# Kernel optimization log

Measured on AMD Instinct MI355X. Metric: run time of the kernel, lower is better.

## Reference

```python
import jax, jax.numpy as jnp
import numpy as np

N_SAMPLES = 32768
N_MESH = 8
N_VERTS = 50000
N_CHAN = 256
N_LEVELS = 6
DEPTH_VIEW = 2
DEPTH_ALPHA = 2
VIEW_DIM = 3 * 2 * N_LEVELS  # 36


def sincos_embed(x, n_levels):
    # x: (..., 3) -> (..., 3*2*n_levels), ordered [sin(f0*x), cos(f0*x), sin(f1*x), ...]
    freqs = (2.0 ** jnp.arange(n_levels, dtype=x.dtype))  # (L,)
    xf = x[..., None, :] * freqs[:, None]                 # (..., L, 3)
    sc = jnp.stack([jnp.sin(xf), jnp.cos(xf)], axis=-2)   # (..., L, 2, 3)
    return sc.reshape(*x.shape[:-1], n_levels * 2 * 3)


def setup_inputs() -> dict:
    key = jax.random.key(0)
    ks = jax.random.split(key, 20)
    s = N_CHAN ** -0.5
    inp = {
        'verts': jax.random.randint(ks[0], (N_SAMPLES, N_MESH, 3), 0, N_VERTS, dtype=jnp.int64 if jax.config.jax_enable_x64 else jnp.int32),
        'barys': jax.random.uniform(ks[1], (N_SAMPLES, N_MESH, 3), dtype=jnp.float32),
        'views': jax.random.normal(ks[2], (N_SAMPLES, N_MESH, 3), dtype=jnp.float32),
        'emb_tables': jax.random.normal(ks[3], (N_MESH, N_VERTS + 1, N_CHAN), dtype=jnp.float32) * s,
        'w_proj': jax.random.normal(ks[4], (VIEW_DIM, N_CHAN), dtype=jnp.float32) * VIEW_DIM ** -0.5,
        'b_proj': jnp.zeros((N_CHAN,), jnp.float32),
        'view_W': jax.random.normal(ks[5], (DEPTH_VIEW, N_CHAN, N_CHAN), dtype=jnp.float32) * s,
        'view_b': jnp.zeros((DEPTH_VIEW, N_CHAN), jnp.float32),
        'vert_W': jax.random.normal(ks[6], (DEPTH_ALPHA, N_CHAN, N_CHAN), dtype=jnp.float32) * s,
        'vert_b': jnp.zeros((DEPTH_ALPHA, N_CHAN), jnp.float32),
        'alpha_W1': jax.random.normal(ks[7], (N_CHAN, N_CHAN), dtype=jnp.float32) * s,
        'alpha_b1': jnp.zeros((N_CHAN,), jnp.float32),
        'alpha_W2': jax.random.normal(ks[8], (N_CHAN, 1), dtype=jnp.float32) * s,
        'alpha_b2': jnp.zeros((1,), jnp.float32),
        'color_W1': jax.random.normal(ks[9], (2 * N_CHAN, 2 * N_CHAN), dtype=jnp.float32) * (2 * N_CHAN) ** -0.5,
        'color_b1': jnp.zeros((2 * N_CHAN,), jnp.float32),
        'color_W2': jax.random.normal(ks[10], (2 * N_CHAN, 3), dtype=jnp.float32) * (2 * N_CHAN) ** -0.5,
        'color_b2': jnp.zeros((3,), jnp.float32),
    }
    return inp


def reference(verts, barys, views, emb_tables, w_proj, b_proj, view_W, view_b,
              vert_W, vert_b, alpha_W1, alpha_b1, alpha_W2, alpha_b2,
              color_W1, color_b1, color_W2, color_b2):
    idx = verts + 1                                   # (N, M, 3); row 0 reserved
    mesh_ids = jnp.arange(N_MESH)[None, :, None]      # (1, M, 1)
    ve = emb_tables[mesh_ids, idx]                    # (N, M, 3, C) per-mesh gather
    # nn.Embedding max_norm=1.0: renormalize gathered rows with L2 norm > 1
    norm = jnp.linalg.norm(ve, axis=-1, keepdims=True)
    ve = ve * jnp.where(norm > 1.0, 1.0 / jnp.maximum(norm, 1e-7), 1.0)
    # barycentric-weighted sum over the 3 triangle vertices
    vertex_embeds = jnp.einsum('nmv,nmvc->nmc', barys, ve)  # (N, M, C)

    # view branch: sincos -> linear projector -> Linear+ReLU stack
    v = sincos_embed(views, N_LEVELS) @ w_proj + b_proj
    for i in range(DEPTH_VIEW):
        v = jax.nn.relu(v @ view_W[i] + view_b[i])

    # alpha branch: Linear+ReLU stack then identity-activation head
    h = vertex_embeds
    for i in range(DEPTH_ALPHA):
        h = jax.nn.relu(h @ vert_W[i] + vert_b[i])
    alphas = (h @ alpha_W1 + alpha_b1) @ alpha_W2 + alpha_b2  # (N, M, 1)

    # color branch on [view_embed, vertex_embeds], identity activations
    c = jnp.concatenate([v, vertex_embeds], axis=-1)          # (N, M, 2C)
    colors = (c @ color_W1 + color_b1) @ color_W2 + color_b2  # (N, M, 3)

    return jnp.concatenate([colors, alphas], axis=-1)         # (N, M, 4)
```

## Files before the change

kernel.cpp:

```cpp
#include <hip/hip_runtime.h>
#include <math.h>


#define NROWS (32768 * 8)
#define VROWS 50001
#define BM 32

typedef unsigned short u16;
typedef unsigned int u32;
typedef __attribute__((ext_vector_type(8))) short s16x8;
typedef __attribute__((ext_vector_type(4))) float f32x4;

#define MFMA(a, b, c) __builtin_amdgcn_mfma_f32_16x16x32_bf16(a, b, c, 0, 0, 0)

#define WF_OFF 0
#define BL0_OFF 16384
#define AEFF_OFF 16640
#define CEFFT_OFF 16896
#define BA_OFF 18432
#define BC_OFF 18433
#define PK_FLOAT_OFF 18560
#define L0H 0
#define L0L 16384
#define L1H 32768
#define L1L 98304
#define L2H 163840
#define L2L 229376
#define L3H 294912
#define L3L 360448
#define L4H 425984
#define L4L 430080

__device__ __forceinline__ u16 btrunc(float x) { return (u16)(__float_as_uint(x) >> 16); }
__device__ __forceinline__ u16 bround(float x) {
  u32 u = __float_as_uint(x);
  u += 0x7fff + ((u >> 16) & 1);
  return (u16)(u >> 16);
}

__global__ void mc_prep(const float* w_proj, const float* b_proj, const float* view_W,
                        const float* view_b, const float* alpha_W1, const float* alpha_b1,
                        const float* alpha_W2, const float* alpha_b2, const float* color_W1,
                        const float* color_b1, const float* color_W2, const float* color_b2,
                        float* ws) {
  int bid = blockIdx.x, tid = threadIdx.x;
  if (bid < 64) {
    int k = bid, n = tid;
    float s = 0.f;
    if (k < 36)
      for (int j = 0; j < 256; ++j) s = fmaf(w_proj[k * 256 + j], view_W[j * 256 + n], s);
    ws[WF_OFF + k * 256 + n] = s;
  } else if (bid == 64) {
    int n = tid;
    float s = view_b[n];
    for (int j = 0; j < 256; ++j) s = fmaf(b_proj[j], view_W[j * 256 + n], s);
    ws[BL0_OFF + n] = s;
  } else if (bid == 65) {
    int k = tid;
    float s = 0.f;
    for (int j = 0; j < 256; ++j) s = fmaf(alpha_W1[k * 256 + j], alpha_W2[j], s);
    ws[AEFF_OFF + k] = s;
    if (tid == 0) {
      float b = alpha_b2[0];
      for (int j = 0; j < 256; ++j) b = fmaf(alpha_b1[j], alpha_W2[j], b);
      ws[BA_OFF] = b;
    }
  } else {
    int kk = (bid - 66) * 256 + tid;
    for (int c = 0; c < 3; ++c) {
      float s = 0.f;
      for (int j = 0; j < 512; ++j) s = fmaf(color_W1[kk * 512 + j], color_W2[j * 3 + c], s);
      ws[CEFFT_OFF + c * 512 + kk] = s;
    }
    if (bid == 66 && tid == 0) {
      for (int c = 0; c < 3; ++c) {
        float s = color_b2[c];
        for (int j = 0; j < 512; ++j) s = fmaf(color_b1[j], color_W2[j * 3 + c], s);
        ws[BC_OFF + c] = s;
      }
    }
  }
}

__global__ void mc_pack(const float* view_W, const float* vert_W, const float* ws_f, u16* pk) {
  int e = blockIdx.x * 256 + threadIdx.x;
  float x;
  int offh, offl, le;
  if (e < 212992) {
    const float* src;
    int KS;
    if (e < 16384) {
      src = ws_f + WF_OFF; KS = 2; offh = L0H; offl = L0L; le = e;
    } else if (e < 81920) {
      src = view_W + 65536; KS = 8; offh = L1H; offl = L1L; le = e - 16384;
    } else if (e < 147456) {
      src = vert_W; KS = 8; offh = L2H; offl = L2L; le = e - 81920;
    } else {
      src = vert_W + 65536; KS = 8; offh = L3H; offl = L3L; le = e - 147456;
    }
    int j = le & 7, lane = (le >> 3) & 63, rest = le >> 9;
    int ks = rest % KS, at = rest / KS;
    int k = ks * 32 + ((lane >> 4) << 3) + j;
    int n = at * 16 + (lane & 15);
    x = src[k * 256 + n];
  } else {
    le = e - 212992;
    offh = L4H; offl = L4L;
    int j = le & 7, lane = (le >> 3) & 63, ks = le >> 9;
    int k = ks * 32 + ((lane >> 4) << 3) + j;
    int c = lane & 15;
    x = (c < 3) ? ws_f[CEFFT_OFF + c * 512 + 256 + k] : 0.f;
  }
  u16 h = btrunc(x);
  float r = x - __uint_as_float(((u32)h) << 16);
  pk[offh + le] = h;
  pk[offl + le] = btrunc(r);
}

template <int KS, int AS, bool EXTRA, bool BLO>
__device__ __forceinline__ void run_gemm(const u16* Bh, const u16* Bl, const u16* pk,
                                         int offh, int offl, int wid, int lane,
                                         f32x4 (&acc)[4][2], f32x4* accx) {
#pragma unroll
  for (int ks = 0; ks < KS; ++ks) {
    s16x8 b_h[2], b_l[2];
#pragma unroll
    for (int rt = 0; rt < 2; ++rt) {
      int row = rt * 16 + (lane & 15);
      u32 byte = (u32)(row * AS + ks * 64 + ((lane >> 4) << 4));
      byte ^= ((u32)(row & 7) << 4);
      b_h[rt] = *(const s16x8*)((const char*)Bh + byte);
      if (BLO) b_l[rt] = *(const s16x8*)((const char*)Bl + byte);
    }
#pragma unroll
    for (int atl = 0; atl < 4; ++atl) {
      int at = wid * 4 + atl;
      size_t fidx = ((size_t)(at * KS + ks) * 64 + lane) * 8;
      s16x8 a_h = *(const s16x8*)(pk + offh + fidx);
      s16x8 a_l = *(const s16x8*)(pk + offl + fidx);
#pragma unroll
      for (int rt = 0; rt < 2; ++rt) {
        acc[atl][rt] = MFMA(a_h, b_h[rt], acc[atl][rt]);
        if (BLO) acc[atl][rt] = MFMA(a_h, b_l[rt], acc[atl][rt]);
        acc[atl][rt] = MFMA(a_l, b_h[rt], acc[atl][rt]);
      }
    }
    if (EXTRA) {
      if ((ks >> 1) == wid) {
        size_t fx = ((size_t)ks * 64 + lane) * 8;
        s16x8 ax_h = *(const s16x8*)(pk + L4H + fx);
        s16x8 ax_l = *(const s16x8*)(pk + L4L + fx);
#pragma unroll
        for (int rt = 0; rt < 2; ++rt) {
          accx[rt] = MFMA(ax_h, b_h[rt], accx[rt]);
          if (BLO) accx[rt] = MFMA(ax_h, b_l[rt], accx[rt]);
          accx[rt] = MFMA(ax_l, b_h[rt], accx[rt]);
        }
      }
    }
  }
}

__device__ __forceinline__ void zero_acc(f32x4 (&acc)[4][2]) {
#pragma unroll
  for (int a = 0; a < 4; ++a)
#pragma unroll
    for (int r = 0; r < 2; ++r) acc[a][r] = (f32x4){0.f, 0.f, 0.f, 0.f};
}

__device__ __forceinline__ void store_relu(const f32x4 (&acc)[4][2], const float* bias,
                                           u16* Oh, u16* Ol, int wid, int lane) {
  const int lg = (lane >> 4) << 2;
#pragma unroll
  for (int atl = 0; atl < 4; ++atl) {
    int nb = (wid * 4 + atl) * 16 + lg;
    f32x4 bv = *(const f32x4*)(bias + nb);
#pragma unroll
    for (int rt = 0; rt < 2; ++rt) {
      int row = rt * 16 + (lane & 15);
      u32 byte = (u32)(row * 512 + nb * 2);
      byte ^= ((u32)(row & 7) << 4);
      float v0 = acc[atl][rt][0] + bv[0]; v0 = v0 > 0.f ? v0 : 0.f;
      float v1 = acc[atl][rt][1] + bv[1]; v1 = v1 > 0.f ? v1 : 0.f;
      float v2 = acc[atl][rt][2] + bv[2]; v2 = v2 > 0.f ? v2 : 0.f;
      float v3 = acc[atl][rt][3] + bv[3]; v3 = v3 > 0.f ? v3 : 0.f;
      ushort4 h, l;
      float r;
      h.x = btrunc(v0); r = v0 - __uint_as_float(((u32)h.x) << 16); l.x = btrunc(r);
      h.y = btrunc(v1); r = v1 - __uint_as_float(((u32)h.y) << 16); l.y = btrunc(r);
      h.z = btrunc(v2); r = v2 - __uint_as_float(((u32)h.z) << 16); l.z = btrunc(r);
      h.w = btrunc(v3); r = v3 - __uint_as_float(((u32)h.w) << 16); l.w = btrunc(r);
      *(ushort4*)((char*)Oh + byte) = h;
      *(ushort4*)((char*)Ol + byte) = l;
    }
  }
}

__global__ __launch_bounds__(256, 4) void mc_main(const int* __restrict__ verts,
                                                  const float* __restrict__ barys,
                                                  const float* __restrict__ views,
                                                  const float* __restrict__ emb_tables,
                                                  const float* __restrict__ view_b,
                                                  const float* __restrict__ vert_b,
                                                  const float* __restrict__ ws_f,
                                                  const u16* __restrict__ pk,
                                                  float* __restrict__ out) {
  __shared__ u16 ACTh[BM * 256], ACTl[BM * 256];
  __shared__ u16 Eh[BM * 64];
  __shared__ float cpart[4][BM][3];
  __shared__ float apart[4][BM];

  const int tid = threadIdx.x, lane = tid & 63, wid = tid >> 6;
  const int rbase = blockIdx.x * BM;

  for (int p = 0; p < 4; ++p) {
    const int row0 = wid * 8 + p * 2;
    float4 val[2][3];
    float bw[2][3];
#pragma unroll
    for (int r = 0; r < 2; ++r) {
      const int R = rbase + row0 + r;
      const int m = R & 7;
#pragma unroll
      for (int v = 0; v < 3; ++v) {
        int idx = verts[R * 3 + v] + 1;
        bw[r][v] = barys[R * 3 + v];
        val[r][v] = ((const float4*)(emb_tables + ((size_t)m * VROWS + idx) * 256))[lane];
      }
    }
    float ss[2][3];
#pragma unroll
    for (int r = 0; r < 2; ++r)
#pragma unroll
      for (int v = 0; v < 3; ++v)
        ss[r][v] = fmaf(val[r][v].x, val[r][v].x,
                   fmaf(val[r][v].y, val[r][v].y,
                   fmaf(val[r][v].z, val[r][v].z, val[r][v].w * val[r][v].w)));
#pragma unroll
    for (int sh = 1; sh < 64; sh <<= 1) {
#pragma unroll
      for (int r = 0; r < 2; ++r)
#pragma unroll
        for (int v = 0; v < 3; ++v) ss[r][v] += __shfl_xor(ss[r][v], sh);
    }
#pragma unroll
    for (int r = 0; r < 2; ++r) {
      float ax = 0.f, ay = 0.f, az = 0.f, aw = 0.f;
#pragma unroll
      for (int v = 0; v < 3; ++v) {
        float norm = sqrtf(ss[r][v]);
        float scale = norm > 1.f ? 1.f / norm : 1.f;
        float wbs = bw[r][v] * scale;
        ax = fmaf(wbs, val[r][v].x, ax);
        ay = fmaf(wbs, val[r][v].y, ay);
        az = fmaf(wbs, val[r][v].z, az);
        aw = fmaf(wbs, val[r][v].w, aw);
      }
      const int row = row0 + r;
      u32 byte = (u32)(row * 512 + lane * 8);
      byte ^= ((u32)(row & 7) << 4);
      ushort4 h, l;
      float rr;
      h.x = btrunc(ax); rr = ax - __uint_as_float(((u32)h.x) << 16); l.x = btrunc(rr);
      h.y = btrunc(ay); rr = ay - __uint_as_float(((u32)h.y) << 16); l.y = btrunc(rr);
      h.z = btrunc(az); rr = az - __uint_as_float(((u32)h.z) << 16); l.z = btrunc(rr);
      h.w = btrunc(aw); rr = aw - __uint_as_float(((u32)h.w) << 16); l.w = btrunc(rr);
      *(ushort4*)((char*)ACTh + byte) = h;
      *(ushort4*)((char*)ACTl + byte) = l;
    }
  }

  {
    const int row = tid >> 3, slot = tid & 7;
    const int R = rbase + row;
    if (slot < 6) {
      float f = (float)(1 << slot);
#pragma unroll
      for (int d = 0; d < 3; ++d) {
        float x = views[R * 3 + d] * f;
        float s, c;
        sincosf(x, &s, &c);
        u32 b1 = ((u32)(row * 128 + (slot * 6 + d) * 2)) ^ ((u32)(row & 7) << 4);
        u32 b2 = ((u32)(row * 128 + (slot * 6 + 3 + d) * 2)) ^ ((u32)(row & 7) << 4);
        *(u16*)((char*)Eh + b1) = bround(s);
        *(u16*)((char*)Eh + b2) = bround(c);
      }
    } else {
      int c0 = 36 + (slot - 6) * 14;
      for (int c = c0; c < c0 + 14; ++c) {
        u32 b = ((u32)(row * 128 + c * 2)) ^ ((u32)(row & 7) << 4);
        *(u16*)((char*)Eh + b) = 0;
      }
    }
  }
  __syncthreads();

  {
    f32x4 acc[4][2], accx[2];
    zero_acc(acc);
    accx[0] = (f32x4){0.f, 0.f, 0.f, 0.f};
    accx[1] = (f32x4){0.f, 0.f, 0.f, 0.f};
    run_gemm<8, 512, true, true>(ACTh, ACTl, pk, L2H, L2L, wid, lane, acc, accx);
    if ((lane >> 4) == 0) {
#pragma unroll
      for (int rt = 0; rt < 2; ++rt)
#pragma unroll
        for (int c = 0; c < 3; ++c) cpart[wid][rt * 16 + lane][c] = accx[rt][c];
    }
    __syncthreads();
    store_relu(acc, vert_b, ACTh, ACTl, wid, lane);
  }
  __syncthreads();

  {
    f32x4 acc[4][2];
    zero_acc(acc);
    run_gemm<8, 512, false, true>(ACTh, ACTl, pk, L3H, L3L, wid, lane, acc, nullptr);
    const int lg = (lane >> 4) << 2;
    float s[2] = {0.f, 0.f};
#pragma unroll
    for (int atl = 0; atl < 4; ++atl) {
      int nb = (wid * 4 + atl) * 16 + lg;
      f32x4 bv = *(const f32x4*)(vert_b + 256 + nb);
      f32x4 av = *(const f32x4*)(ws_f + AEFF_OFF + nb);
#pragma unroll
      for (int rt = 0; rt < 2; ++rt)
#pragma unroll
        for (int reg = 0; reg < 4; ++reg) {
          float v = acc[atl][rt][reg] + bv[reg];
          v = v > 0.f ? v : 0.f;
          s[rt] = fmaf(v, av[reg], s[rt]);
        }
    }
#pragma unroll
    for (int rt = 0; rt < 2; ++rt) {
      s[rt] += __shfl_xor(s[rt], 16);
      s[rt] += __shfl_xor(s[rt], 32);
    }
    if (lane < 16) {
      apart[wid][lane] = s[0];
      apart[wid][16 + lane] = s[1];
    }
  }
  __syncthreads();

  {
    f32x4 acc[4][2];
    zero_acc(acc);
    run_gemm<2, 128, false, false>(Eh, Eh, pk, L0H, L0L, wid, lane, acc, nullptr);
    store_relu(acc, ws_f + BL0_OFF, ACTh, ACTl, wid, lane);
  }
  __syncthreads();

  {
    f32x4 acc[4][2];
    zero_acc(acc);
    run_gemm<8, 512, false, true>(ACTh, ACTl, pk, L1H, L1L, wid, lane, acc, nullptr);
    const int lg = (lane >> 4) << 2;
    float s[2][3] = {{0.f, 0.f, 0.f}, {0.f, 0.f, 0.f}};
#pragma unroll
    for (int atl = 0; atl < 4; ++atl) {
      int nb = (wid * 4 + atl) * 16 + lg;
      f32x4 bv = *(const f32x4*)(view_b + 256 + nb);
      f32x4 w0 = *(const f32x4*)(ws_f + CEFFT_OFF + 0 * 512 + nb);
      f32x4 w1 = *(const f32x4*)(ws_f + CEFFT_OFF + 1 * 512 + nb);
      f32x4 w2 = *(const f32x4*)(ws_f + CEFFT_OFF + 2 * 512 + nb);
#pragma unroll
      for (int rt = 0; rt < 2; ++rt)
#pragma unroll
        for (int reg = 0; reg < 4; ++reg) {
          float v = acc[atl][rt][reg] + bv[reg];
          v = v > 0.f ? v : 0.f;
          s[rt][0] = fmaf(v, w0[reg], s[rt][0]);
          s[rt][1] = fmaf(v, w1[reg], s[rt][1]);
          s[rt][2] = fmaf(v, w2[reg], s[rt][2]);
        }
    }
#pragma unroll
    for (int rt = 0; rt < 2; ++rt)
#pragma unroll
      for (int c = 0; c < 3; ++c) {
        s[rt][c] += __shfl_xor(s[rt][c], 16);
        s[rt][c] += __shfl_xor(s[rt][c], 32);
      }
    if (lane < 16) {
#pragma unroll
      for (int rt = 0; rt < 2; ++rt)
#pragma unroll
        for (int c = 0; c < 3; ++c) cpart[wid][rt * 16 + lane][c] += s[rt][c];
    }
  }
  __syncthreads();

  if (tid < BM * 4) {
    int row = tid >> 2, c = tid & 3;
    float v;
    if (c < 3) {
      v = cpart[0][row][c] + cpart[1][row][c] + cpart[2][row][c] + cpart[3][row][c] +
          ws_f[BC_OFF + c];
    } else {
      v = apart[0][row] + apart[1][row] + apart[2][row] + apart[3][row] + ws_f[BA_OFF];
    }
    out[(size_t)(rbase + row) * 4 + c] = v;
  }
}

extern "C" void kernel_launch(void* const* d_in, const int* in_sizes, int n_in, void* d_out,
                              int out_size, void* d_ws, size_t ws_size, hipStream_t stream) {
  (void)in_sizes; (void)n_in; (void)out_size; (void)ws_size;
  const int* verts = (const int*)d_in[0];
  const float* barys = (const float*)d_in[1];
  const float* views = (const float*)d_in[2];
  const float* emb_tables = (const float*)d_in[3];
  const float* w_proj = (const float*)d_in[4];
  const float* b_proj = (const float*)d_in[5];
  const float* view_W = (const float*)d_in[6];
  const float* view_b = (const float*)d_in[7];
  const float* vert_W = (const float*)d_in[8];
  const float* vert_b = (const float*)d_in[9];
  const float* alpha_W1 = (const float*)d_in[10];
  const float* alpha_b1 = (const float*)d_in[11];
  const float* alpha_W2 = (const float*)d_in[12];
  const float* alpha_b2 = (const float*)d_in[13];
  const float* color_W1 = (const float*)d_in[14];
  const float* color_b1 = (const float*)d_in[15];
  const float* color_W2 = (const float*)d_in[16];
  const float* color_b2 = (const float*)d_in[17];

  float* ws_f = (float*)d_ws;
  u16* pk = (u16*)(ws_f + PK_FLOAT_OFF);

  mc_prep<<<dim3(68), dim3(256), 0, stream>>>(w_proj, b_proj, view_W, view_b, alpha_W1,
                                              alpha_b1, alpha_W2, alpha_b2, color_W1, color_b1,
                                              color_W2, color_b2, ws_f);
  mc_pack<<<dim3(848), dim3(256), 0, stream>>>(view_W, vert_W, ws_f, pk);
  mc_main<<<dim3(NROWS / BM), dim3(256), 0, stream>>>(verts, barys, views, emb_tables, view_b,
                                                      vert_b, ws_f, pk, (float*)d_out);
}
```

Measured before the change: 983.2 us.

## Double row tile to 64 with 8 waves, batch gathers, atomic LDS reductions

Raises the row tile from 32 to 64 rows and runs 8 waves per block. Each wave now covers 2 output column tiles across 4 row tiles, so every packed weight fragment fetched from global memory is reused across twice as many rows. The embedding gather is restructured to issue 12 loads per batch in two batches, with the sincos encoding placed between them to hide load latency. The per-wave partial sums for color and alpha are replaced by LDS atomicAdd into a single buffer. The trade-offs are higher register pressure under launch bounds of 512 threads, a larger LDS footprint per block and atomic contention in LDS.

```diff
diff --git a/kernel.cpp b/kernel.cpp
--- a/kernel.cpp
+++ b/kernel.cpp
@@ -4,7 +4,8 @@
 
 #define NROWS (32768 * 8)
 #define VROWS 50001
-#define BM 32
+#define BM 64
+#define NW 8
 
 typedef unsigned short u16;
 typedef unsigned int u32;
@@ -120,12 +121,12 @@
 template <int KS, int AS, bool EXTRA, bool BLO>
 __device__ __forceinline__ void run_gemm(const u16* Bh, const u16* Bl, const u16* pk,
                                          int offh, int offl, int wid, int lane,
-                                         f32x4 (&acc)[4][2], f32x4* accx) {
+                                         f32x4 (&acc)[2][4], f32x4* accx) {
 #pragma unroll
   for (int ks = 0; ks < KS; ++ks) {
-    s16x8 b_h[2], b_l[2];
-#pragma unroll
-    for (int rt = 0; rt < 2; ++rt) {
+    s16x8 b_h[4], b_l[4];
+#pragma unroll
+    for (int rt = 0; rt < 4; ++rt) {
       int row = rt * 16 + (lane & 15);
       u32 byte = (u32)(row * AS + ks * 64 + ((lane >> 4) << 4));
       byte ^= ((u32)(row & 7) << 4);
@@ -133,25 +134,25 @@
       if (BLO) b_l[rt] = *(const s16x8*)((const char*)Bl + byte);
     }
 #pragma unroll
-    for (int atl = 0; atl < 4; ++atl) {
-      int at = wid * 4 + atl;
+    for (int atl = 0; atl < 2; ++atl) {
+      int at = wid * 2 + atl;
       size_t fidx = ((size_t)(at * KS + ks) * 64 + lane) * 8;
       s16x8 a_h = *(const s16x8*)(pk + offh + fidx);
       s16x8 a_l = *(const s16x8*)(pk + offl + fidx);
 #pragma unroll
-      for (int rt = 0; rt < 2; ++rt) {
+      for (int rt = 0; rt < 4; ++rt) {
         acc[atl][rt] = MFMA(a_h, b_h[rt], acc[atl][rt]);
         if (BLO) acc[atl][rt] = MFMA(a_h, b_l[rt], acc[atl][rt]);
         acc[atl][rt] = MFMA(a_l, b_h[rt], acc[atl][rt]);
       }
     }
     if (EXTRA) {
-      if ((ks >> 1) == wid) {
+      if (ks == wid) {
         size_t fx = ((size_t)ks * 64 + lane) * 8;
         s16x8 ax_h = *(const s16x8*)(pk + L4H + fx);
         s16x8 ax_l = *(const s16x8*)(pk + L4L + fx);
 #pragma unroll
-        for (int rt = 0; rt < 2; ++rt) {
+        for (int rt = 0; rt < 4; ++rt) {
           accx[rt] = MFMA(ax_h, b_h[rt], accx[rt]);
           if (BLO) accx[rt] = MFMA(ax_h, b_l[rt], accx[rt]);
           accx[rt] = MFMA(ax_l, b_h[rt], accx[rt]);
@@ -161,22 +162,22 @@
   }
 }
 
-__device__ __forceinline__ void zero_acc(f32x4 (&acc)[4][2]) {
-#pragma unroll
-  for (int a = 0; a < 4; ++a)
-#pragma unroll
-    for (int r = 0; r < 2; ++r) acc[a][r] = (f32x4){0.f, 0.f, 0.f, 0.f};
-}
-
-__device__ __forceinline__ void store_relu(const f32x4 (&acc)[4][2], const float* bias,
+__device__ __forceinline__ void zero_acc(f32x4 (&acc)[2][4]) {
+#pragma unroll
+  for (int a = 0; a < 2; ++a)
+#pragma unroll
+    for (int r = 0; r < 4; ++r) acc[a][r] = (f32x4){0.f, 0.f, 0.f, 0.f};
+}
+
+__device__ __forceinline__ void store_relu(const f32x4 (&acc)[2][4], const float* bias,
                                            u16* Oh, u16* Ol, int wid, int lane) {
   const int lg = (lane >> 4) << 2;
 #pragma unroll
-  for (int atl = 0; atl < 4; ++atl) {
-    int nb = (wid * 4 + atl) * 16 + lg;
+  for (int atl = 0; atl < 2; ++atl) {
+    int nb = (wid * 2 + atl) * 16 + lg;
     f32x4 bv = *(const f32x4*)(bias + nb);
 #pragma unroll
-    for (int rt = 0; rt < 2; ++rt) {
+    for (int rt = 0; rt < 4; ++rt) {
       int row = rt * 16 + (lane & 15);
       u32 byte = (u32)(row * 512 + nb * 2);
       byte ^= ((u32)(row & 7) << 4);
@@ -196,7 +197,7 @@
   }
 }
 
-__global__ __launch_bounds__(256, 4) void mc_main(const int* __restrict__ verts,
+__global__ __launch_bounds__(512, 4) void mc_main(const int* __restrict__ verts,
                                                   const float* __restrict__ barys,
                                                   const float* __restrict__ views,
                                                   const float* __restrict__ emb_tables,
@@ -207,105 +208,127 @@
                                                   float* __restrict__ out) {
   __shared__ u16 ACTh[BM * 256], ACTl[BM * 256];
   __shared__ u16 Eh[BM * 64];
-  __shared__ float cpart[4][BM][3];
-  __shared__ float apart[4][BM];
+  __shared__ float cpart[BM * 4];
 
   const int tid = threadIdx.x, lane = tid & 63, wid = tid >> 6;
   const int rbase = blockIdx.x * BM;
 
-  for (int p = 0; p < 4; ++p) {
-    const int row0 = wid * 8 + p * 2;
-    float4 val[2][3];
-    float bw[2][3];
-#pragma unroll
-    for (int r = 0; r < 2; ++r) {
-      const int R = rbase + row0 + r;
-      const int m = R & 7;
+  if (tid < BM * 4) cpart[tid] = 0.f;
+
+  {
+    const int r0 = wid * 8;
+    int idxs[8][3];
+    float bws[8][3];
+#pragma unroll
+    for (int r = 0; r < 8; ++r)
 #pragma unroll
       for (int v = 0; v < 3; ++v) {
-        int idx = verts[R * 3 + v] + 1;
-        bw[r][v] = barys[R * 3 + v];
-        val[r][v] = ((const float4*)(emb_tables + ((size_t)m * VROWS + idx) * 256))[lane];
-      }
-    }
-    float ss[2][3];
-#pragma unroll
-    for (int r = 0; r < 2; ++r)
+        const int R = rbase + r0 + r;
+        idxs[r][v] = verts[R * 3 + v] + 1;
+        bws[r][v] = barys[R * 3 + v];
+      }
+    float4 valA[4][3];
+#pragma unroll
+    for (int r = 0; r < 4; ++r) {
+      const int m = (rbase + r0 + r) & 7;
 #pragma unroll
       for (int v = 0; v < 3; ++v)
-        ss[r][v] = fmaf(val[r][v].x, val[r][v].x,
-                   fmaf(val[r][v].y, val[r][v].y,
-                   fmaf(val[r][v].z, val[r][v].z, val[r][v].w * val[r][v].w)));
-#pragma unroll
-    for (int sh = 1; sh < 64; sh <<= 1) {
-#pragma unroll
-      for (int r = 0; r < 2; ++r)
-#pragma unroll
-        for (int v = 0; v < 3; ++v) ss[r][v] += __shfl_xor(ss[r][v], sh);
-    }
-#pragma unroll
-    for (int r = 0; r < 2; ++r) {
-      float ax = 0.f, ay = 0.f, az = 0.f, aw = 0.f;
-#pragma unroll
-      for (int v = 0; v < 3; ++v) {
-        float norm = sqrtf(ss[r][v]);
-        float scale = norm > 1.f ? 1.f / norm : 1.f;
-        float wbs = bw[r][v] * scale;
-        ax = fmaf(wbs, val[r][v].x, ax);
-        ay = fmaf(wbs, val[r][v].y, ay);
-        az = fmaf(wbs, val[r][v].z, az);
-        aw = fmaf(wbs, val[r][v].w, aw);
-      }
-      const int row = row0 + r;
-      u32 byte = (u32)(row * 512 + lane * 8);
-      byte ^= ((u32)(row & 7) << 4);
-      ushort4 h, l;
-      float rr;
-      h.x = btrunc(ax); rr = ax - __uint_as_float(((u32)h.x) << 16); l.x = btrunc(rr);
-      h.y = btrunc(ay); rr = ay - __uint_as_float(((u32)h.y) << 16); l.y = btrunc(rr);
-      h.z = btrunc(az); rr = az - __uint_as_float(((u32)h.z) << 16); l.z = btrunc(rr);
-      h.w = btrunc(aw); rr = aw - __uint_as_float(((u32)h.w) << 16); l.w = btrunc(rr);
-      *(ushort4*)((char*)ACTh + byte) = h;
-      *(ushort4*)((char*)ACTl + byte) = l;
-    }
-  }
+        valA[r][v] =
+            ((const float4*)(emb_tables + ((size_t)m * VROWS + idxs[r][v]) * 256))[lane];
+    }
+
+    {
+      const int row = tid >> 3, slot = tid & 7;
+      const int R = rbase + row;
+      if (slot < 6) {
+        float f = (float)(1 << slot);
+#pragma unroll
+        for (int d = 0; d < 3; ++d) {
+          float x = views[R * 3 + d] * f;
+          float s, c;
+          sincosf(x, &s, &c);
+          u32 b1 = ((u32)(row * 128 + (slot * 6 + d) * 2)) ^ ((u32)(row & 7) << 4);
+          u32 b2 = ((u32)(row * 128 + (slot * 6 + 3 + d) * 2)) ^ ((u32)(row & 7) << 4);
+          *(u16*)((char*)Eh + b1) = bround(s);
+          *(u16*)((char*)Eh + b2) = bround(c);
+        }
+      } else {
+        int c0 = 36 + (slot - 6) * 14;
+        for (int c = c0; c < c0 + 14; ++c) {
+          u32 b = ((u32)(row * 128 + c * 2)) ^ ((u32)(row & 7) << 4);
+          *(u16*)((char*)Eh + b) = 0;
+        }
+      }
+    }
+
+    float4 valB[4][3];
+#pragma unroll
+    for (int r = 0; r < 4; ++r) {
+      const int m = (rbase + r0 + 4 + r) & 7;
+#pragma unroll
+      for (int v = 0; v < 3; ++v)
+        valB[r][v] =
+            ((const float4*)(emb_tables + ((size_t)m * VROWS + idxs[4 + r][v]) * 256))[lane];
+    }
+
+#define CONSUME(VAL, RBASE_R)                                                                \
+    {                                                                                        \
+      float ss[4][3];                                                                        \
+      _Pragma("unroll") for (int r = 0; r < 4; ++r) _Pragma("unroll") for (int v = 0; v < 3; \
+                                                                           ++v) ss[r][v] =   \
+          fmaf(VAL[r][v].x, VAL[r][v].x,                                                     \
+               fmaf(VAL[r][v].y, VAL[r][v].y,                                                \
+                    fmaf(VAL[r][v].z, VAL[r][v].z, VAL[r][v].w * VAL[r][v].w)));             \
+      _Pragma("unroll") for (int sh = 1; sh < 64; sh <<= 1) {                                \
+        _Pragma("unroll") for (int r = 0; r < 4; ++r) _Pragma("unroll") for (int v = 0;      \
+                                                                             v < 3; ++v)     \
+            ss[r][v] += __shfl_xor(ss[r][v], sh);                                            \
+      }                                                                                      \
+      _Pragma("unroll") for (int r = 0; r < 4; ++r) {                                        \
+        float ax = 0.f, ay = 0.f, az = 0.f, aw = 0.f;                                        \
+        _Pragma("unroll") for (int v = 0; v < 3; ++v) {                                      \
+          float norm = sqrtf(ss[r][v]);                                                      \
+          float scale = norm > 1.f ? 1.f / norm : 1.f;                                       \
+          float wbs = bws[RBASE_R][v] * scale;                                               \
+          ax = fmaf(wbs, VAL[r][v].x, ax);                                                   \
+          ay = fmaf(wbs, VAL[r][v].y, ay);                                                   \
+          az = fmaf(wbs, VAL[r][v].z, az);                                                   \
+          aw = fmaf(wbs, VAL[r][v].w, aw);                                                   \
+        }                                                                                    \
+        const int row = r0 + (RBASE_R);                                                      \
+        u32 byte = (u32)(row * 512 + lane * 8);                                              \
+        byte ^= ((u32)(row & 7) << 4);                                                       \
+        ushort4 h, l;                                                                        \
+        float rr;                                                                            \
+        h.x = btrunc(ax); rr = ax - __uint_as_float(((u32)h.x) << 16); l.x = btrunc(rr);     \
+        h.y = btrunc(ay); rr = ay - __uint_as_float(((u32)h.y) << 16); l.y = btrunc(rr);     \
+        h.z = btrunc(az); rr = az - __uint_as_float(((u32)h.z) << 16); l.z = btrunc(rr);     \
+        h.w = btrunc(aw); rr = aw - __uint_as_float(((u32)h.w) << 16); l.w = btrunc(rr);     \
+        *(ushort4*)((char*)ACTh + byte) = h;                                                 \
+        *(ushort4*)((char*)ACTl + byte) = l;                                                 \
+      }                                                                                      \
+    }
+
+    CONSUME(valA, r)
+#define RPLUS4 (r + 4)
+    CONSUME(valB, RPLUS4)
+#undef RPLUS4
+#undef CONSUME
+  }
+  __syncthreads();
 
   {
-    const int row = tid >> 3, slot = tid & 7;
-    const int R = rbase + row;
-    if (slot < 6) {
-      float f = (float)(1 << slot);
-#pragma unroll
-      for (int d = 0; d < 3; ++d) {
-        float x = views[R * 3 + d] * f;
-        float s, c;
-        sincosf(x, &s, &c);
-        u32 b1 = ((u32)(row * 128 + (slot * 6 + d) * 2)) ^ ((u32)(row & 7) << 4);
-        u32 b2 = ((u32)(row * 128 + (slot * 6 + 3 + d) * 2)) ^ ((u32)(row & 7) << 4);
-        *(u16*)((char*)Eh + b1) = bround(s);
-        *(u16*)((char*)Eh + b2) = bround(c);
-      }
-    } else {
-      int c0 = 36 + (slot - 6) * 14;
-      for (int c = c0; c < c0 + 14; ++c) {
-        u32 b = ((u32)(row * 128 + c * 2)) ^ ((u32)(row & 7) << 4);
-        *(u16*)((char*)Eh + b) = 0;
-      }
-    }
-  }
-  __syncthreads();
-
-  {
-    f32x4 acc[4][2], accx[2];
+    f32x4 acc[2][4], accx[4];
     zero_acc(acc);
-    accx[0] = (f32x4){0.f, 0.f, 0.f, 0.f};
-    accx[1] = (f32x4){0.f, 0.f, 0.f, 0.f};
+#pragma unroll
+    for (int rt = 0; rt < 4; ++rt) accx[rt] = (f32x4){0.f, 0.f, 0.f, 0.f};
     run_gemm<8, 512, true, true>(ACTh, ACTl, pk, L2H, L2L, wid, lane, acc, accx);
-    if ((lane >> 4) == 0) {
-#pragma unroll
-      for (int rt = 0; rt < 2; ++rt)
-#pragma unroll
-        for (int c = 0; c < 3; ++c) cpart[wid][rt * 16 + lane][c] = accx[rt][c];
+    if (lane < 16) {
+#pragma unroll
+      for (int rt = 0; rt < 4; ++rt)
+#pragma unroll
+        for (int c = 0; c < 3; ++c)
+          atomicAdd(&cpart[(rt * 16 + lane) * 4 + c], accx[rt][c]);
     }
     __syncthreads();
     store_relu(acc, vert_b, ACTh, ACTl, wid, lane);
@@ -313,18 +336,18 @@
   __syncthreads();
 
   {
-    f32x4 acc[4][2];
+    f32x4 acc[2][4];
     zero_acc(acc);
     run_gemm<8, 512, false, true>(ACTh, ACTl, pk, L3H, L3L, wid, lane, acc, nullptr);
     const int lg = (lane >> 4) << 2;
-    float s[2] = {0.f, 0.f};
-#pragma unroll
-    for (int atl = 0; atl < 4; ++atl) {
-      int nb = (wid * 4 + atl) * 16 + lg;
+    float s[4] = {0.f, 0.f, 0.f, 0.f};
+#pragma unroll
+    for (int atl = 0; atl < 2; ++atl) {
+      int nb = (wid * 2 + atl) * 16 + lg;
       f32x4 bv = *(const f32x4*)(vert_b + 256 + nb);
       f32x4 av = *(const f32x4*)(ws_f + AEFF_OFF + nb);
 #pragma unroll
-      for (int rt = 0; rt < 2; ++rt)
+      for (int rt = 0; rt < 4; ++rt)
 #pragma unroll
         for (int reg = 0; reg < 4; ++reg) {
           float v = acc[atl][rt][reg] + bv[reg];
@@ -333,19 +356,19 @@
         }
     }
 #pragma unroll
-    for (int rt = 0; rt < 2; ++rt) {
+    for (int rt = 0; rt < 4; ++rt) {
       s[rt] += __shfl_xor(s[rt], 16);
       s[rt] += __shfl_xor(s[rt], 32);
     }
     if (lane < 16) {
-      apart[wid][lane] = s[0];
-      apart[wid][16 + lane] = s[1];
+#pragma unroll
+      for (int rt = 0; rt < 4; ++rt) atomicAdd(&cpart[(rt * 16 + lane) * 4 + 3], s[rt]);
     }
   }
   __syncthreads();
 
   {
-    f32x4 acc[4][2];
+    f32x4 acc[2][4];
     zero_acc(acc);
     run_gemm<2, 128, false, false>(Eh, Eh, pk, L0H, L0L, wid, lane, acc, nullptr);
     store_relu(acc, ws_f + BL0_OFF, ACTh, ACTl, wid, lane);
@@ -353,20 +376,24 @@
   __syncthreads();
 
   {
-    f32x4 acc[4][2];
+    f32x4 acc[2][4];
     zero_acc(acc);
     run_gemm<8, 512, false, true>(ACTh, ACTl, pk, L1H, L1L, wid, lane, acc, nullptr);
     const int lg = (lane >> 4) << 2;
-    float s[2][3] = {{0.f, 0.f, 0.f}, {0.f, 0.f, 0.f}};
-#pragma unroll
-    for (int atl = 0; atl < 4; ++atl) {
-      int nb = (wid * 4 + atl) * 16 + lg;
+    float s[4][3];
+#pragma unroll
+    for (int rt = 0; rt < 4; ++rt)
+#pragma unroll
+      for (int c = 0; c < 3; ++c) s[rt][c] = 0.f;
+#pragma unroll
+    for (int atl = 0; atl < 2; ++atl) {
+      int nb = (wid * 2 + atl) * 16 + lg;
       f32x4 bv = *(const f32x4*)(view_b + 256 + nb);
       f32x4 w0 = *(const f32x4*)(ws_f + CEFFT_OFF + 0 * 512 + nb);
       f32x4 w1 = *(const f32x4*)(ws_f + CEFFT_OFF + 1 * 512 + nb);
       f32x4 w2 = *(const f32x4*)(ws_f + CEFFT_OFF + 2 * 512 + nb);
 #pragma unroll
-      for (int rt = 0; rt < 2; ++rt)
+      for (int rt = 0; rt < 4; ++rt)
 #pragma unroll
         for (int reg = 0; reg < 4; ++reg) {
           float v = acc[atl][rt][reg] + bv[reg];
@@ -377,7 +404,7 @@
         }
     }
 #pragma unroll
-    for (int rt = 0; rt < 2; ++rt)
+    for (int rt = 0; rt < 4; ++rt)
 #pragma unroll
       for (int c = 0; c < 3; ++c) {
         s[rt][c] += __shfl_xor(s[rt][c], 16);
@@ -385,23 +412,18 @@
       }
     if (lane < 16) {
 #pragma unroll
-      for (int rt = 0; rt < 2; ++rt)
-#pragma unroll
-        for (int c = 0; c < 3; ++c) cpart[wid][rt * 16 + lane][c] += s[rt][c];
+      for (int rt = 0; rt < 4; ++rt)
+#pragma unroll
+        for (int c = 0; c < 3; ++c)
+          atomicAdd(&cpart[(rt * 16 + lane) * 4 + c], s[rt][c]);
     }
   }
   __syncthreads();
 
   if (tid < BM * 4) {
-    int row = tid >> 2, c = tid & 3;
-    float v;
-    if (c < 3) {
-      v = cpart[0][row][c] + cpart[1][row][c] + cpart[2][row][c] + cpart[3][row][c] +
-          ws_f[BC_OFF + c];
-    } else {
-      v = apart[0][row] + apart[1][row] + apart[2][row] + apart[3][row] + ws_f[BA_OFF];
-    }
-    out[(size_t)(rbase + row) * 4 + c] = v;
+    int c = tid & 3;
+    float v = cpart[tid] + (c < 3 ? ws_f[BC_OFF + c] : ws_f[BA_OFF]);
+    out[(size_t)rbase * 4 + tid] = v;
   }
 }
 
@@ -434,6 +456,6 @@
                                               alpha_b1, alpha_W2, alpha_b2, color_W1, color_b1,
                                               color_W2, color_b2, ws_f);
   mc_pack<<<dim3(848), dim3(256), 0, stream>>>(view_W, vert_W, ws_f, pk);
-  mc_main<<<dim3(NROWS / BM), dim3(256), 0, stream>>>(verts, barys, views, emb_tables, view_b,
+  mc_main<<<dim3(NROWS / BM), dim3(512), 0, stream>>>(verts, barys, views, emb_tables, view_b,
                                                       vert_b, ws_f, pk, (float*)d_out);
 }
```

Result: slower. 1.035 ms (+5.2%).
